# Kernel tuning notes

Measured on AMD Instinct MI355X. Metric: run time of the kernel, lower is better.

## Reference

```python
import math
import jax, jax.numpy as jnp
import numpy as np

D_MODEL = 1024
HEADS = 16
DH = D_MODEL // HEADS
MAX_REL = 128
LN_EPS = 1e-5


def setup_inputs() -> dict:
    key = jax.random.key(0)
    ks = jax.random.split(key, 6)
    B, T = 4, 2048
    scale = 1.0 / math.sqrt(D_MODEL)
    x = jax.random.normal(ks[0], (B, T, D_MODEL), dtype=jnp.float32)
    Wq = jax.random.normal(ks[1], (D_MODEL, D_MODEL), dtype=jnp.float32) * scale
    Wk = jax.random.normal(ks[2], (D_MODEL, D_MODEL), dtype=jnp.float32) * scale
    Wv = jax.random.normal(ks[3], (D_MODEL, D_MODEL), dtype=jnp.float32) * scale
    Wo = jax.random.normal(ks[4], (D_MODEL, D_MODEL), dtype=jnp.float32) * scale
    # rel bias init as in torch: per-head linspace(0, -2, max_rel+1)
    rel = jnp.tile(jnp.linspace(0.0, -2.0, MAX_REL + 1, dtype=jnp.float32)[None, :], (HEADS, 1))
    ln_gamma = jnp.ones((D_MODEL,), dtype=jnp.float32)
    ln_beta = jnp.zeros((D_MODEL,), dtype=jnp.float32)
    return {"x": x, "Wq": Wq, "Wk": Wk, "Wv": Wv, "Wo": Wo,
            "rel": rel, "ln_gamma": ln_gamma, "ln_beta": ln_beta}


def _layernorm(x, gamma, beta):
    mu = jnp.mean(x, axis=-1, keepdims=True)
    var = jnp.mean(jnp.square(x - mu), axis=-1, keepdims=True)
    return (x - mu) * jax.lax.rsqrt(var + LN_EPS) * gamma + beta


def reference(x, Wq, Wk, Wv, Wo, rel, ln_gamma, ln_beta):
    B, T, D = x.shape
    x0 = x
    xn = _layernorm(x, ln_gamma, ln_beta)
    # projections -> [B, H, T, dh]  (torch Linear: x @ W.T; weights here stored as [out,in])
    def proj(W):
        return (xn @ W.T).reshape(B, T, HEADS, DH).transpose(0, 2, 1, 3)
    q = proj(Wq) / math.sqrt(DH)
    k = proj(Wk)
    v = proj(Wv)
    scores = jnp.einsum('bhid,bhjd->bhij', q, k)  # [B,H,T,T]
    # latency-aware relative bias: bias[h,i,j] = rel[h, min(max(i-j,0), max_rel)]
    i = jnp.arange(T)
    dist = jnp.clip(i[:, None] - i[None, :], 0, MAX_REL)  # [T,T]
    bias = rel[:, dist]  # [H,T,T]
    scores = scores + bias[None]
    causal = i[:, None] >= i[None, :]  # j <= i allowed
    scores = jnp.where(causal[None, None], scores, -jnp.inf)
    attn = jax.nn.softmax(scores, axis=-1)
    y = jnp.einsum('bhij,bhjd->bhid', attn, v)  # [B,H,T,dh]
    y = y.transpose(0, 2, 1, 3).reshape(B, T, D)
    y = y @ Wo.T
    return x0 + y
```

## Files before the change

kernel.cpp:

```cpp
#include <hip/hip_runtime.h>
#include <math.h>

#define TSEQ 2048
#define BATCH 4
#define NH 16
#define DH 64
#define DM 1024
#define NREL 129
#define NEGBIG (-1.0e30f)
#define FIXMAX 8.0f

typedef unsigned short u16;
typedef unsigned int u32;
typedef __attribute__((ext_vector_type(8))) short bf16x8;
typedef __attribute__((ext_vector_type(4))) float f32x4;
typedef __attribute__((ext_vector_type(4))) unsigned short u16x4;

typedef __attribute__((address_space(3))) void lds_void;
typedef const __attribute__((address_space(1))) void g_void;

__device__ inline u16 f2b(float f) {
    union { float f; u32 i; } c; c.f = f;
    u32 x = c.i;
    return (u16)((x + 0x7fffu + ((x >> 16) & 1u)) >> 16);
}

__device__ inline u32 cvtpk(float lo, float hi) {
    u32 r;
    asm("v_cvt_pk_bf16_f32 %0, %1, %2" : "=v"(r) : "v"(lo), "v"(hi));
    return r;
}

__global__ __launch_bounds__(256) void fill_kernel(float* __restrict__ out, int n, float v) {
    for (int i = blockIdx.x * 256 + threadIdx.x; i < n; i += gridDim.x * 256)
        out[i] = v;
}

__global__ __launch_bounds__(256) void ln_kernel(const float* __restrict__ x,
        const float* __restrict__ gamma, const float* __restrict__ beta,
        u16* __restrict__ xn) {
    const int row = blockIdx.x;
    const int tid = threadIdx.x;
    const float* xr = x + (size_t)row * DM;
    f32x4 xv = *(const f32x4*)(xr + tid * 4);
    float s = xv.x + xv.y + xv.z + xv.w;
    float s2 = xv.x*xv.x + xv.y*xv.y + xv.z*xv.z + xv.w*xv.w;
#pragma unroll
    for (int off = 32; off > 0; off >>= 1) {
        s  += __shfl_down(s, off, 64);
        s2 += __shfl_down(s2, off, 64);
    }
    __shared__ alignas(16) float red[8];
    const int wv = tid >> 6, ln = tid & 63;
    if (ln == 0) { red[wv] = s; red[4 + wv] = s2; }
    __syncthreads();
    s  = red[0] + red[1] + red[2] + red[3];
    s2 = red[4] + red[5] + red[6] + red[7];
    const float mu = s * (1.0f / DM);
    float var = s2 * (1.0f / DM) - mu * mu;
    var = var > 0.0f ? var : 0.0f;
    const float rstd = rsqrtf(var + 1e-5f);
    f32x4 gv = *(const f32x4*)(gamma + tid * 4);
    f32x4 bv = *(const f32x4*)(beta + tid * 4);
    u16x4 ov;
    ov.x = f2b((xv.x - mu) * rstd * gv.x + bv.x);
    ov.y = f2b((xv.y - mu) * rstd * gv.y + bv.y);
    ov.z = f2b((xv.z - mu) * rstd * gv.z + bv.z);
    ov.w = f2b((xv.w - mu) * rstd * gv.w + bv.w);
    *(u16x4*)(xn + (size_t)row * DM + tid * 4) = ov;
}

__global__ __launch_bounds__(256) void cvt3_kernel(const float* __restrict__ a,
        const float* __restrict__ b, const float* __restrict__ c,
        u16* __restrict__ dst) {
    const int i = blockIdx.x * 256 + threadIdx.x;
    const int m = i >> 18;
    const int j = i & 0x3FFFF;
    const float* src = m == 0 ? a : (m == 1 ? b : c);
    const float scale = m == 0 ? 0.125f : 1.0f;
    f32x4 v = *(const f32x4*)(src + (size_t)j * 4);
    u16x4 o;
    o.x = f2b(v.x * scale); o.y = f2b(v.y * scale);
    o.z = f2b(v.z * scale); o.w = f2b(v.w * scale);
    *(u16x4*)(dst + (size_t)i * 4) = o;
}

__global__ __launch_bounds__(256) void cvt1_kernel(const float* __restrict__ src,
        u16* __restrict__ dst, int n4) {
    const int i = blockIdx.x * 256 + threadIdx.x;
    if (i >= n4) return;
    f32x4 v = *(const f32x4*)(src + (size_t)i * 4);
    u16x4 o;
    o.x = f2b(v.x); o.y = f2b(v.y); o.z = f2b(v.z); o.w = f2b(v.w);
    *(u16x4*)(dst + (size_t)i * 4) = o;
}

#define BM 128
#define BN 128
#define BK 32

__global__ __launch_bounds__(256) void gemm_qkv(const u16* __restrict__ A,
        const u16* __restrict__ W3, u16* __restrict__ Qb, u16* __restrict__ Kb,
        u16* __restrict__ Vb) {
    __shared__ alignas(16) u16 sh[16384];
    const int id = blockIdx.x + 64 * blockIdx.y;
    const int xcd = id & 7;
    const int k = id >> 3;
    const int xv = xcd * 8 + (k & 7);
    const int yv = k >> 3;
    const int m0 = xv * BM;
    const int mat = yv >> 3;
    const int n0 = (yv & 7) * BN;
    const u16* Wb = W3 + (size_t)mat * DM * DM;
    const int tid = threadIdx.x;
    const int w = tid >> 6;
    const int lane = tid & 63;
    const int quad = lane >> 4, l16 = lane & 15;
    const int wr = (w >> 1) * 64;
    const int wc = (w & 1) * 64;

    const int c0 = w * 2;
    const int srow = c0 * 16 + (lane >> 2);
    const int scol = (((lane & 3) ^ ((lane >> 3) & 3))) * 8;
    const u16* ag = A  + (size_t)(m0 + srow) * DM + scol;
    const u16* bg = Wb + (size_t)(n0 + srow) * DM + scol;
    u16* asw = sh + c0 * 512;
    u16* bsw = sh + 8192 + c0 * 512;
    const int sx = (quad ^ ((l16 >> 1) & 3)) * 8;

    f32x4 acc[4][4];
#pragma unroll
    for (int i = 0; i < 4; i++)
#pragma unroll
        for (int j = 0; j < 4; j++) acc[i][j] = (f32x4){0.f, 0.f, 0.f, 0.f};

#define QKV_STAGE(buf, kk) do { \
    __builtin_amdgcn_global_load_lds((g_void*)(ag + (kk)),            (lds_void*)(asw + (buf)*4096),       16, 0, 0); \
    __builtin_amdgcn_global_load_lds((g_void*)(ag + (kk) + 16 * DM),  (lds_void*)(asw + (buf)*4096 + 512), 16, 0, 0); \
    __builtin_amdgcn_global_load_lds((g_void*)(bg + (kk)),            (lds_void*)(bsw + (buf)*4096),       16, 0, 0); \
    __builtin_amdgcn_global_load_lds((g_void*)(bg + (kk) + 16 * DM),  (lds_void*)(bsw + (buf)*4096 + 512), 16, 0, 0); \
} while (0)

    QKV_STAGE(0, 0);
    __syncthreads();
    for (int k0 = 0; k0 < DM; k0 += BK) {
        const int cur = (k0 >> 5) & 1;
        if (k0 + BK < DM) QKV_STAGE(cur ^ 1, k0 + BK);
        const u16* Ac = sh + cur * 4096;
        const u16* Bc = sh + 8192 + cur * 4096;
        bf16x8 af[4], bfr[4];
#pragma unroll
        for (int mt = 0; mt < 4; mt++)
            af[mt] = *(const bf16x8*)(Ac + (wr + mt * 16 + l16) * BK + sx);
#pragma unroll
        for (int nt = 0; nt < 4; nt++)
            bfr[nt] = *(const bf16x8*)(Bc + (wc + nt * 16 + l16) * BK + sx);
#pragma unroll
        for (int mt = 0; mt < 4; mt++)
#pragma unroll
            for (int nt = 0; nt < 4; nt++)
                acc[mt][nt] = __builtin_amdgcn_mfma_f32_16x16x32_bf16(af[mt], bfr[nt], acc[mt][nt], 0, 0, 0);
        __syncthreads();
    }
#undef QKV_STAGE

    u16* outb = mat == 0 ? Qb : (mat == 1 ? Kb : Vb);
    const size_t bh = (size_t)(m0 >> 11) * NH + ((n0 + wc) >> 6);
    const int tq = (m0 & 2047) + wr;
    u16* stage = sh + w * 2048;

#pragma unroll
    for (int p = 0; p < 2; p++) {
#pragma unroll
        for (int mt = 0; mt < 4; mt++) {
#pragma unroll
            for (int ntl = 0; ntl < 2; ntl++) {
                const int nt = p * 2 + ntl;
#pragma unroll
                for (int r = 0; r < 4; r++) {
                    const u16 val = f2b(acc[mt][nt][r]);
                    int a;
                    if (mat == 0) {
                        a = mt * 512
                          + ((ntl * 2 + (l16 >> 3)) * 16 + quad * 4 + r) * 8 + (l16 & 7);
                    } else if (mat == 1) {
                        a = ((mt >> 1) * 2 + (quad & 1)) * 512
                          + ((ntl * 2 + (l16 >> 3)) * 16 + (quad >> 1) * 4 + (mt & 1) * 8 + r) * 8
                          + (l16 & 7);
                    } else {
                        a = ((mt >> 1) * 2 + ntl) * 512
                          + (((mt * 2 + (quad >> 1)) & 3) * 16 + l16) * 8
                          + (quad & 1) * 4 + r;
                    }
                    stage[a] = val;
                }
            }
        }
#pragma unroll
        for (int c = 0; c < 4; c++) {
            const bf16x8 vv = *(const bf16x8*)(stage + c * 512 + lane * 8);
            size_t gc;
            if (mat == 0)      gc = (bh * 128 + (tq >> 4) + c) * 2 + p;
            else if (mat == 1) gc = (bh * 64 + (tq >> 5) + (c >> 1)) * 4 + (c & 1) * 2 + p;
            else               gc = (bh * 64 + (tq >> 5) + (c >> 1)) * 4 + p * 2 + (c & 1);
            *(bf16x8*)(outb + gc * 512 + lane * 8) = vv;
        }
    }
}

__global__ __launch_bounds__(256) void gemm_wo(const u16* __restrict__ A,
        const u16* __restrict__ Wb, const float* __restrict__ X0,
        float* __restrict__ out) {
    __shared__ alignas(16) u16 sh[16384];
    const int id = blockIdx.x + 64 * blockIdx.y;
    const int xcd = id & 7;
    const int k = id >> 3;
    const int m0 = (xcd * 8 + (k & 7)) * BM;
    const int n0 = (k >> 3) * BN;
    const int tid = threadIdx.x;
    const int w = tid >> 6;
    const int lane = tid & 63;
    const int quad = lane >> 4, l16 = lane & 15;
    const int wr = (w >> 1) * 64;
    const int wc = (w & 1) * 64;

    const int c0 = w * 2;
    const int srow = c0 * 16 + (lane >> 2);
    const int scol = (((lane & 3) ^ ((lane >> 3) & 3))) * 8;
    const u16* ag = A  + (size_t)(m0 + srow) * DM + scol;
    const u16* bg = Wb + (size_t)(n0 + srow) * DM + scol;
    u16* asw = sh + c0 * 512;
    u16* bsw = sh + 8192 + c0 * 512;
    const int sx = (quad ^ ((l16 >> 1) & 3)) * 8;

    f32x4 acc[4][4];
#pragma unroll
    for (int i = 0; i < 4; i++)
#pragma unroll
        for (int j = 0; j < 4; j++) acc[i][j] = (f32x4){0.f, 0.f, 0.f, 0.f};

#define WO_STAGE(buf, kk) do { \
    __builtin_amdgcn_global_load_lds((g_void*)(ag + (kk)),            (lds_void*)(asw + (buf)*4096),       16, 0, 0); \
    __builtin_amdgcn_global_load_lds((g_void*)(ag + (kk) + 16 * DM),  (lds_void*)(asw + (buf)*4096 + 512), 16, 0, 0); \
    __builtin_amdgcn_global_load_lds((g_void*)(bg + (kk)),            (lds_void*)(bsw + (buf)*4096),       16, 0, 0); \
    __builtin_amdgcn_global_load_lds((g_void*)(bg + (kk) + 16 * DM),  (lds_void*)(bsw + (buf)*4096 + 512), 16, 0, 0); \
} while (0)

    WO_STAGE(0, 0);
    __syncthreads();
    for (int k0 = 0; k0 < DM; k0 += BK) {
        const int cur = (k0 >> 5) & 1;
        if (k0 + BK < DM) WO_STAGE(cur ^ 1, k0 + BK);
        const u16* Ac = sh + cur * 4096;
        const u16* Bc = sh + 8192 + cur * 4096;
        bf16x8 af[4], bfr[4];
#pragma unroll
        for (int mt = 0; mt < 4; mt++)
            af[mt] = *(const bf16x8*)(Ac + (wr + mt * 16 + l16) * BK + sx);
#pragma unroll
        for (int nt = 0; nt < 4; nt++)
            bfr[nt] = *(const bf16x8*)(Bc + (wc + nt * 16 + l16) * BK + sx);
#pragma unroll
        for (int mt = 0; mt < 4; mt++)
#pragma unroll
            for (int nt = 0; nt < 4; nt++)
                acc[mt][nt] = __builtin_amdgcn_mfma_f32_16x16x32_bf16(af[mt], bfr[nt], acc[mt][nt], 0, 0, 0);
        __syncthreads();
    }
#undef WO_STAGE

#pragma unroll
    for (int mt = 0; mt < 4; mt++) {
#pragma unroll
        for (int nt = 0; nt < 4; nt++) {
#pragma unroll
            for (int r = 0; r < 4; r++) {
                const int row = m0 + wr + mt * 16 + quad * 4 + r;
                const int col = n0 + wc + nt * 16 + l16;
                const size_t idx = (size_t)row * DM + col;
                out[idx] = acc[mt][nt][r] + X0[idx];
            }
        }
    }
}

__device__ inline bf16x8 sm_pack(f32x4 s0, f32x4 s1, int dq, bool fast,
                                 const float* rel_s, float r128) {
    float p0[4], p1[4];
    if (fast) {
#pragma unroll
        for (int r = 0; r < 4; r++) {
            p0[r] = __expf(s0[r] + (r128 - FIXMAX));
            p1[r] = __expf(s1[r] + (r128 - FIXMAX));
        }
    } else {
#pragma unroll
        for (int r = 0; r < 4; r++) {
            const int d0 = dq - r;
            const int d1 = dq - 4 - r;
            const int c0 = d0 < 0 ? 0 : (d0 > 128 ? 128 : d0);
            const int c1 = d1 < 0 ? 0 : (d1 > 128 ? 128 : d1);
            float sv0 = s0[r] + rel_s[c0];
            float sv1 = s1[r] + rel_s[c1];
            sv0 = d0 >= 0 ? sv0 : NEGBIG;
            sv1 = d1 >= 0 ? sv1 : NEGBIG;
            p0[r] = __expf(sv0 - FIXMAX);
            p1[r] = __expf(sv1 - FIXMAX);
        }
    }
    union { u32 u[4]; bf16x8 v; } pk_;
    pk_.u[0] = cvtpk(p0[0], p0[1]);
    pk_.u[1] = cvtpk(p0[2], p0[3]);
    pk_.u[2] = cvtpk(p1[0], p1[1]);
    pk_.u[3] = cvtpk(p1[2], p1[3]);
    return pk_.v;
}

__global__ __launch_bounds__(512, 4) void attn_kernel(const u16* __restrict__ Q,
        const u16* __restrict__ K, const u16* __restrict__ Vt,
        const float* __restrict__ rel, u16* __restrict__ y) {
    const int id = blockIdx.x + 8 * blockIdx.y;
    const int xcd = id & 7;
    const int idx = id >> 3;
    const int bh = xcd * 8 + (idx & 7);
    const int p = idx >> 3;
    const int h = bh & (NH - 1);
    const int b = bh >> 4;
    const int tid = threadIdx.x;
    const int w = tid >> 6, lane = tid & 63;
    const int rg = w & 3, jg = w >> 2;
    const int quad = lane >> 4, l16 = lane & 15;

    __shared__ alignas(16) float rel_s[NREL];
    __shared__ alignas(16) f32x4 cb[4][2][5][64];
    __shared__ alignas(16) u16 st_s[4][1024];
    if (tid < NREL) rel_s[tid] = rel[h * NREL + tid];
    __syncthreads();
    const float r128 = rel_s[128];

    const u16* Qh = Q  + (size_t)bh * TSEQ * DH;
    const u16* Kh = K  + (size_t)bh * TSEQ * DH;
    const u16* Vh = Vt + (size_t)bh * TSEQ * DH;

    bf16x8 ones;
#pragma unroll
    for (int j = 0; j < 8; j++) ones[j] = (short)0x3F80;

    for (int ti = 0; ti < 2; ti++) {
        const int qt = ti ? (15 - p) : p;
        const int lo = qt * 128 + rg * 32;
        const int hi = lo + 16;
        const int gqL = lo + l16, gqH = hi + l16;
        const u16* qb = Qh + (size_t)(lo >> 4) * 1024 + lane * 8;
        const bf16x8 qf0L = *(const bf16x8*)(qb);
        const bf16x8 qf1L = *(const bf16x8*)(qb + 512);
        const bf16x8 qf0H = *(const bf16x8*)(qb + 1024);
        const bf16x8 qf1H = *(const bf16x8*)(qb + 1536);

        f32x4 o0[4], o1[4];
#pragma unroll
        for (int i = 0; i < 4; i++) {
            o0[i] = (f32x4){0.f, 0.f, 0.f, 0.f};
            o1[i] = (f32x4){0.f, 0.f, 0.f, 0.f};
        }
        f32x4 l0 = (f32x4){0.f, 0.f, 0.f, 0.f};
        f32x4 l1 = (f32x4){0.f, 0.f, 0.f, 0.f};

        for (int j0 = jg * 32; j0 < lo + 32; j0 += 64) {
            const u16* kb = Kh + (size_t)(j0 >> 5) * 2048 + lane * 8;
            const bf16x8 k00 = *(const bf16x8*)(kb);
            const bf16x8 k01 = *(const bf16x8*)(kb + 512);
            const bf16x8 k10 = *(const bf16x8*)(kb + 1024);
            const bf16x8 k11 = *(const bf16x8*)(kb + 1536);
            const bool doLo = j0 < hi;

            f32x4 sH0 = (f32x4){0.f, 0.f, 0.f, 0.f};
            f32x4 sH1 = (f32x4){0.f, 0.f, 0.f, 0.f};
            sH0 = __builtin_amdgcn_mfma_f32_16x16x32_bf16(k00, qf0H, sH0, 0, 0, 0);
            sH0 = __builtin_amdgcn_mfma_f32_16x16x32_bf16(k01, qf1H, sH0, 0, 0, 0);
            sH1 = __builtin_amdgcn_mfma_f32_16x16x32_bf16(k10, qf0H, sH1, 0, 0, 0);
            sH1 = __builtin_amdgcn_mfma_f32_16x16x32_bf16(k11, qf1H, sH1, 0, 0, 0);
            f32x4 sL0 = (f32x4){0.f, 0.f, 0.f, 0.f};
            f32x4 sL1 = (f32x4){0.f, 0.f, 0.f, 0.f};
            if (doLo) {
                sL0 = __builtin_amdgcn_mfma_f32_16x16x32_bf16(k00, qf0L, sL0, 0, 0, 0);
                sL0 = __builtin_amdgcn_mfma_f32_16x16x32_bf16(k01, qf1L, sL0, 0, 0, 0);
                sL1 = __builtin_amdgcn_mfma_f32_16x16x32_bf16(k10, qf0L, sL1, 0, 0, 0);
                sL1 = __builtin_amdgcn_mfma_f32_16x16x32_bf16(k11, qf1L, sL1, 0, 0, 0);
            }

            const bf16x8 pfH = sm_pack(sH0, sH1, gqH - j0 - 8 * quad,
                                       j0 + 159 < hi, rel_s, r128);
            bf16x8 pfL = pfH;
            if (doLo)
                pfL = sm_pack(sL0, sL1, gqL - j0 - 8 * quad,
                              j0 + 159 < lo, rel_s, r128);

            const u16* vb = Vh + (size_t)(j0 >> 5) * 2048 + lane * 8;
            bf16x8 vf[4];
#pragma unroll
            for (int dt = 0; dt < 4; dt++)
                vf[dt] = *(const bf16x8*)(vb + dt * 512);
#pragma unroll
            for (int dt = 0; dt < 4; dt++)
                o1[dt] = __builtin_amdgcn_mfma_f32_16x16x32_bf16(pfH, vf[dt], o1[dt], 0, 0, 0);
            l1 = __builtin_amdgcn_mfma_f32_16x16x32_bf16(pfH, ones, l1, 0, 0, 0);
            if (doLo) {
#pragma unroll
                for (int dt = 0; dt < 4; dt++)
                    o0[dt] = __builtin_amdgcn_mfma_f32_16x16x32_bf16(pfL, vf[dt], o0[dt], 0, 0, 0);
                l0 = __builtin_amdgcn_mfma_f32_16x16x32_bf16(pfL, ones, l0, 0, 0, 0);
            }
        }

        if (jg == 1) {
#pragma unroll
            for (int dt = 0; dt < 4; dt++) {
                cb[rg][0][dt][lane] = o0[dt];
                cb[rg][1][dt][lane] = o1[dt];
            }
            cb[rg][0][4][lane] = l0;
            cb[rg][1][4][lane] = l1;
        }
        __syncthreads();
        if (jg == 0) {
#define FINISH(G, OG, LG, BASE) do {                                         \
            _Pragma("unroll")                                                \
            for (int dt = 0; dt < 4; dt++) {                                 \
                const f32x4 op = cb[rg][G][dt][lane];                        \
                OG[dt].x += op.x; OG[dt].y += op.y;                          \
                OG[dt].z += op.z; OG[dt].w += op.w;                          \
            }                                                                \
            const f32x4 lp = cb[rg][G][4][lane];                             \
            LG.x += lp.x; LG.y += lp.y; LG.z += lp.z; LG.w += lp.w;          \
            float inv[4];                                                    \
            _Pragma("unroll")                                                \
            for (int r = 0; r < 4; r++) inv[r] = 1.0f / LG[r];               \
            u16* st = st_s[rg];                                              \
            _Pragma("unroll")                                                \
            for (int dt = 0; dt < 4; dt++)                                   \
                _Pragma("unroll")                                            \
                for (int r = 0; r < 4; r++)                                  \
                    st[(quad * 4 + r) * 64 + dt * 16 + l16] =                \
                        f2b(OG[dt][r] * inv[r]);                             \
            _Pragma("unroll")                                                \
            for (int ps = 0; ps < 2; ps++) {                                 \
                const bf16x8 vv = *(const bf16x8*)(st + ps * 512 + lane * 8);\
                const int row = (BASE) + ps * 8 + (lane >> 3);               \
                *(bf16x8*)(y + ((size_t)(b * TSEQ + row)) * DM + h * DH      \
                           + (lane & 7) * 8) = vv;                           \
            }                                                                \
        } while (0)
            FINISH(0, o0, l0, lo);
            FINISH(1, o1, l1, hi);
#undef FINISH
        }
        __syncthreads();
    }
}

extern "C" void kernel_launch(void* const* d_in, const int* in_sizes, int n_in,
                              void* d_out, int out_size, void* d_ws, size_t ws_size,
                              hipStream_t stream) {
    const float* x   = (const float*)d_in[0];
    const float* Wq  = (const float*)d_in[1];
    const float* Wk  = (const float*)d_in[2];
    const float* Wv  = (const float*)d_in[3];
    const float* Wo  = (const float*)d_in[4];
    const float* rel = (const float*)d_in[5];
    const float* gam = (const float*)d_in[6];
    const float* bet = (const float*)d_in[7];
    u16* ws = (u16*)d_ws;
    const size_t SZ = (size_t)BATCH * TSEQ * DM;
    const size_t need_bytes = 4 * SZ * sizeof(u16);

    if (n_in != 8) {
        fill_kernel<<<4096, 256, 0, stream>>>((float*)d_out, out_size, 8000.0f);
        return;
    }
    if (ws_size < need_bytes) {
        fill_kernel<<<4096, 256, 0, stream>>>((float*)d_out, out_size, 9500.0f);
        return;
    }

    u16* xn = ws;
    u16* Qb = ws + SZ;
    u16* Kb = ws + 2 * SZ;
    u16* Vb = ws + 3 * SZ;
    u16* y  = xn;

    u16* wscr = (u16*)d_out;
    const int W4 = (DM * DM) / 4;

    ln_kernel<<<BATCH * TSEQ, 256, 0, stream>>>(x, gam, bet, xn);
    cvt3_kernel<<<3 * W4 / 256, 256, 0, stream>>>(Wq, Wk, Wv, wscr);
    gemm_qkv<<<dim3(BATCH * TSEQ / BM, 24), 256, 0, stream>>>(xn, wscr, Qb, Kb, Vb);
    attn_kernel<<<dim3(8, BATCH * NH), 512, 0, stream>>>(Qb, Kb, Vb, rel, y);
    cvt1_kernel<<<W4 / 256, 256, 0, stream>>>(Wo, Qb, W4);
    gemm_wo<<<dim3(BATCH * TSEQ / BM, DM / BN), 256, 0, stream>>>(y, Qb, x, (float*)d_out);
}
```

Before: 256.9 us.

## Merge LayerNorm with QKV weight cast and enlarge QKV GEMM tile to 256x128

The LayerNorm and the bf16 cast of Wq/Wk/Wv now run in one launch, with the extra blocks handling the weight conversion. This removes one kernel launch and lets the two jobs overlap. The QKV GEMM now uses 512-thread blocks over a 256x128 output tile on a 1D grid of 768 blocks, with an updated XCD-aware block mapping and a larger LDS buffer. Each staged weight tile is reused across twice as many rows, which cuts B-operand traffic, at the cost of more LDS per block and possibly lower occupancy.

Result: slower. 390.4 us (+52.0%).

```diff
diff --git a/kernel.cpp b/kernel.cpp
--- a/kernel.cpp
+++ b/kernel.cpp
@@ -36,11 +36,26 @@
         out[i] = v;
 }
 
-__global__ __launch_bounds__(256) void ln_kernel(const float* __restrict__ x,
+__global__ __launch_bounds__(256) void lncvt_kernel(const float* __restrict__ x,
         const float* __restrict__ gamma, const float* __restrict__ beta,
-        u16* __restrict__ xn) {
+        u16* __restrict__ xn, const float* __restrict__ wa,
+        const float* __restrict__ wb, const float* __restrict__ wc,
+        u16* __restrict__ wdst) {
+    const int tid = threadIdx.x;
+    if (blockIdx.x >= BATCH * TSEQ) {
+        const int i = (blockIdx.x - BATCH * TSEQ) * 256 + tid;
+        const int m = i >> 18;
+        const int j = i & 0x3FFFF;
+        const float* src = m == 0 ? wa : (m == 1 ? wb : wc);
+        const float scale = m == 0 ? 0.125f : 1.0f;
+        f32x4 v = *(const f32x4*)(src + (size_t)j * 4);
+        u16x4 o;
+        o.x = f2b(v.x * scale); o.y = f2b(v.y * scale);
+        o.z = f2b(v.z * scale); o.w = f2b(v.w * scale);
+        *(u16x4*)(wdst + (size_t)i * 4) = o;
+        return;
+    }
     const int row = blockIdx.x;
-    const int tid = threadIdx.x;
     const float* xr = x + (size_t)row * DM;
     f32x4 xv = *(const f32x4*)(xr + tid * 4);
     float s = xv.x + xv.y + xv.z + xv.w;
@@ -70,21 +85,6 @@
     *(u16x4*)(xn + (size_t)row * DM + tid * 4) = ov;
 }
 
-__global__ __launch_bounds__(256) void cvt3_kernel(const float* __restrict__ a,
-        const float* __restrict__ b, const float* __restrict__ c,
-        u16* __restrict__ dst) {
-    const int i = blockIdx.x * 256 + threadIdx.x;
-    const int m = i >> 18;
-    const int j = i & 0x3FFFF;
-    const float* src = m == 0 ? a : (m == 1 ? b : c);
-    const float scale = m == 0 ? 0.125f : 1.0f;
-    f32x4 v = *(const f32x4*)(src + (size_t)j * 4);
-    u16x4 o;
-    o.x = f2b(v.x * scale); o.y = f2b(v.y * scale);
-    o.z = f2b(v.z * scale); o.w = f2b(v.w * scale);
-    *(u16x4*)(dst + (size_t)i * 4) = o;
-}
-
 __global__ __launch_bounds__(256) void cvt1_kernel(const float* __restrict__ src,
         u16* __restrict__ dst, int n4) {
     const int i = blockIdx.x * 256 + threadIdx.x;
@@ -99,16 +99,16 @@
 #define BN 128
 #define BK 32
 
-__global__ __launch_bounds__(256) void gemm_qkv(const u16* __restrict__ A,
+__global__ __launch_bounds__(512, 6) void gemm_qkv(const u16* __restrict__ A,
         const u16* __restrict__ W3, u16* __restrict__ Qb, u16* __restrict__ Kb,
         u16* __restrict__ Vb) {
-    __shared__ alignas(16) u16 sh[16384];
-    const int id = blockIdx.x + 64 * blockIdx.y;
+    __shared__ alignas(16) u16 sh[24576];
+    const int id = blockIdx.x;
     const int xcd = id & 7;
     const int k = id >> 3;
-    const int xv = xcd * 8 + (k & 7);
-    const int yv = k >> 3;
-    const int m0 = xv * BM;
+    const int xv = xcd * 4 + (k & 3);
+    const int yv = k >> 2;
+    const int m0 = xv * 256;
     const int mat = yv >> 3;
     const int n0 = (yv & 7) * BN;
     const u16* Wb = W3 + (size_t)mat * DM * DM;
@@ -119,13 +119,13 @@
     const int wr = (w >> 1) * 64;
     const int wc = (w & 1) * 64;
 
-    const int c0 = w * 2;
-    const int srow = c0 * 16 + (lane >> 2);
     const int scol = (((lane & 3) ^ ((lane >> 3) & 3))) * 8;
-    const u16* ag = A  + (size_t)(m0 + srow) * DM + scol;
-    const u16* bg = Wb + (size_t)(n0 + srow) * DM + scol;
-    u16* asw = sh + c0 * 512;
-    u16* bsw = sh + 8192 + c0 * 512;
+    const int sra = 32 * w + (lane >> 2);
+    const int srb = 16 * w + (lane >> 2);
+    const u16* ag = A  + (size_t)(m0 + sra) * DM + scol;
+    const u16* bg = Wb + (size_t)(n0 + srb) * DM + scol;
+    u16* asw = sh + w * 1024;
+    u16* bsw = sh + 16384 + w * 512;
     const int sx = (quad ^ ((l16 >> 1) & 3)) * 8;
 
     f32x4 acc[4][4];
@@ -135,10 +135,9 @@
         for (int j = 0; j < 4; j++) acc[i][j] = (f32x4){0.f, 0.f, 0.f, 0.f};
 
 #define QKV_STAGE(buf, kk) do { \
-    __builtin_amdgcn_global_load_lds((g_void*)(ag + (kk)),            (lds_void*)(asw + (buf)*4096),       16, 0, 0); \
-    __builtin_amdgcn_global_load_lds((g_void*)(ag + (kk) + 16 * DM),  (lds_void*)(asw + (buf)*4096 + 512), 16, 0, 0); \
+    __builtin_amdgcn_global_load_lds((g_void*)(ag + (kk)),            (lds_void*)(asw + (buf)*8192),       16, 0, 0); \
+    __builtin_amdgcn_global_load_lds((g_void*)(ag + (kk) + 16 * DM),  (lds_void*)(asw + (buf)*8192 + 512), 16, 0, 0); \
     __builtin_amdgcn_global_load_lds((g_void*)(bg + (kk)),            (lds_void*)(bsw + (buf)*4096),       16, 0, 0); \
-    __builtin_amdgcn_global_load_lds((g_void*)(bg + (kk) + 16 * DM),  (lds_void*)(bsw + (buf)*4096 + 512), 16, 0, 0); \
 } while (0)
 
     QKV_STAGE(0, 0);
@@ -146,8 +145,8 @@
     for (int k0 = 0; k0 < DM; k0 += BK) {
         const int cur = (k0 >> 5) & 1;
         if (k0 + BK < DM) QKV_STAGE(cur ^ 1, k0 + BK);
-        const u16* Ac = sh + cur * 4096;
-        const u16* Bc = sh + 8192 + cur * 4096;
+        const u16* Ac = sh + cur * 8192;
+        const u16* Bc = sh + 16384 + cur * 4096;
         bf16x8 af[4], bfr[4];
 #pragma unroll
         for (int mt = 0; mt < 4; mt++)
@@ -492,9 +491,9 @@
     u16* wscr = (u16*)d_out;
     const int W4 = (DM * DM) / 4;
 
-    ln_kernel<<<BATCH * TSEQ, 256, 0, stream>>>(x, gam, bet, xn);
-    cvt3_kernel<<<3 * W4 / 256, 256, 0, stream>>>(Wq, Wk, Wv, wscr);
-    gemm_qkv<<<dim3(BATCH * TSEQ / BM, 24), 256, 0, stream>>>(xn, wscr, Qb, Kb, Vb);
+    lncvt_kernel<<<BATCH * TSEQ + 3 * W4 / 256, 256, 0, stream>>>(
+        x, gam, bet, xn, Wq, Wk, Wv, wscr);
+    gemm_qkv<<<768, 512, 0, stream>>>(xn, wscr, Qb, Kb, Vb);
     attn_kernel<<<dim3(8, BATCH * NH), 512, 0, stream>>>(Qb, Kb, Vb, rel, y);
     cvt1_kernel<<<W4 / 256, 256, 0, stream>>>(Wo, Qb, W4);
     gemm_wo<<<dim3(BATCH * TSEQ / BM, DM / BN), 256, 0, stream>>>(y, Qb, x, (float*)d_out);
```
